# Kernel optimization log

Hardware: AMD Instinct MI355X
Metric: run time of the kernel (lower is better)

## Reference

```python
import jax, jax.numpy as jnp
import numpy as np

B, L, C = 2, 4096, 1024
H, WIN = 16, 128            # num_heads, window_size (each side)
D = C // H                  # head_dim = 64


def setup_inputs() -> dict:
    key = jax.random.key(0)
    ks = jax.random.split(key, 9)
    s = 0.02
    return {
        "x": jax.random.normal(ks[0], (B, L, C), jnp.float32),
        # Linear weights stored as [in, out] (y = x @ W + b), same math as torch Linear.
        "wq": jax.random.normal(ks[1], (C, C), jnp.float32) * s,
        "bq": jnp.zeros((C,), jnp.float32),
        "wk": jax.random.normal(ks[2], (C, C), jnp.float32) * s,
        "bk": jnp.zeros((C,), jnp.float32),
        "wv": jax.random.normal(ks[3], (C, C), jnp.float32) * s,
        "bv": jnp.zeros((C,), jnp.float32),
        "wo": jax.random.normal(ks[4], (C, C), jnp.float32) * s,
        "bo": jnp.zeros((C,), jnp.float32),
    }


def reference(x, wq, bq, wk, bk, wv, bv, wo, bo):
    b, l, c = x.shape
    nb = l // WIN

    def heads(t):  # (B,L,C) -> (B,H,L,D)
        return t.reshape(b, l, H, D).transpose(0, 2, 1, 3)

    q = heads(x @ wq + bq)
    k = heads(x @ wk + bk)
    v = heads(x @ wv + bv)

    # and ARE included in the softmax, exactly as the original module does).
    kp = jnp.pad(k, ((0, 0), (0, 0), (WIN, WIN), (0, 0)))
    vp = jnp.pad(v, ((0, 0), (0, 0), (WIN, WIN), (0, 0)))

    idx = np.arange(nb)[:, None] * WIN + np.arange(3 * WIN)[None, :]  # [nb, 3W]
    kb = kp[:, :, idx]  # [B,H,nb,3W,D]
    vb = vp[:, :, idx]  # [B,H,nb,3W,D]
    qb = q.reshape(b, H, nb, WIN, D)

    scores = jnp.einsum('bhnqd,bhnkd->bhnqk', qb, kb) / float(np.sqrt(D))
    r = np.arange(WIN)[:, None]
    col = np.arange(3 * WIN)[None, :]
    band = jnp.asarray(np.abs(col - r - WIN) <= WIN)
    scores = jnp.where(band, scores, -jnp.inf)
    probs = jax.nn.softmax(scores, axis=-1)

    out = jnp.einsum('bhnqk,bhnkd->bhnqd', probs, vb)
    out = out.reshape(b, H, l, D).transpose(0, 2, 1, 3).reshape(b, l, c)
    return out @ wo + bo
```

## Files before the change

### kernel.cpp

```cpp
#include <hip/hip_runtime.h>

using short8  = __attribute__((ext_vector_type(8))) short;
using short4v = __attribute__((ext_vector_type(4))) short;
using floatx4 = __attribute__((ext_vector_type(4))) float;

#define MFMA_B16(a, b, c) __builtin_amdgcn_mfma_f32_16x16x32_bf16(a, b, c, 0, 0, 0)

__device__ __forceinline__ short f2bf(float f) {
  union { float f; unsigned u; } v; v.f = f;
  unsigned r = v.u + 0x7fffu + ((v.u >> 16) & 1u);
  return (short)(r >> 16);
}
__device__ __forceinline__ short f2bf_rtz(float f) {
  union { float f; unsigned u; } v; v.f = f;
  return (short)(v.u >> 16);
}

__device__ __forceinline__ void gload_lds16(const short* g, short* l) {
  __builtin_amdgcn_global_load_lds(
      (const __attribute__((address_space(1))) unsigned int*)g,
      (__attribute__((address_space(3))) unsigned int*)l, 16, 0, 0);
}

__global__ __launch_bounds__(256) void prep(
    const float4* __restrict__ x, short4v* __restrict__ xb,
    const float* __restrict__ w0, const float* __restrict__ w1,
    const float* __restrict__ w2, const float* __restrict__ w3,
    short* __restrict__ wT) {
  __shared__ float tile[32][33];
  int blk = blockIdx.x;
  if (blk < 8192) {
    int i = blk * 256 + threadIdx.x;
    float4 v = x[i];
    short4v o = { f2bf(v.x), f2bf(v.y), f2bf(v.z), f2bf(v.w) };
    xb[i] = o;
  } else {
    int r = blk - 8192;
    int z = r >> 10; r &= 1023;
    const float* w = z == 0 ? w0 : (z == 1 ? w1 : (z == 2 ? w2 : w3));
    short* out = wT + (size_t)z * 1024 * 1024;
    int n0 = (r & 31) * 32, k0 = (r >> 5) * 32;
    int tx = threadIdx.x & 31, ty = threadIdx.x >> 5;
#pragma unroll
    for (int i = 0; i < 4; ++i)
      tile[ty + i * 8][tx] = w[(size_t)(k0 + ty + i * 8) * 1024 + n0 + tx];
    __syncthreads();
#pragma unroll
    for (int i = 0; i < 4; ++i)
      out[(size_t)(n0 + ty + i * 8) * 1024 + k0 + tx] = f2bf(tile[tx][ty + i * 8]);
  }
}

__global__ __launch_bounds__(256) void gemm_qkv(
    const short* __restrict__ xb, const short* __restrict__ wT,
    const float* __restrict__ bq, const float* __restrict__ bk,
    const float* __restrict__ bv, short* __restrict__ qkv) {
  const int K = 1024;
  int z = blockIdx.z;
  const short* wt = wT + (size_t)z * 1024 * 1024;
  const float* bias = z == 0 ? bq : (z == 1 ? bk : bv);
  short* out = qkv + (size_t)z * 8192 * 1024;

  int m0 = blockIdx.x * 128, n0 = blockIdx.y * 128;
  __shared__ __align__(16) short a[128][32];
  __shared__ __align__(16) short bt[128][32];
  int tid = threadIdx.x;
  int w = tid >> 6, lane = tid & 63, quad = lane >> 4, l16 = lane & 15;
  int wm = (w >> 1) * 64, wn = (w & 1) * 64;
  floatx4 zf = {0.f, 0.f, 0.f, 0.f};
  floatx4 acc[4][4];
#pragma unroll
  for (int i = 0; i < 4; ++i)
#pragma unroll
    for (int j = 0; j < 4; ++j) acc[i][j] = zf;

  int rowL = lane >> 2;
  int segL = (lane & 3) * 8;
  const short* ga = xb + (size_t)(m0 + w * 32 + rowL) * K + segL;
  const short* gb = wt + (size_t)(n0 + w * 32 + rowL) * K + segL;
  short* la = &a[w * 32][0];
  short* lb = &bt[w * 32][0];

  for (int k0 = 0; k0 < K; k0 += 32) {
    __syncthreads();
    gload_lds16(ga + k0, la);
    gload_lds16(ga + (size_t)16 * K + k0, la + 16 * 32);
    gload_lds16(gb + k0, lb);
    gload_lds16(gb + (size_t)16 * K + k0, lb + 16 * 32);
    __syncthreads();
    short8 af[4], bf[4];
#pragma unroll
    for (int t = 0; t < 4; ++t) {
      af[t] = *(const short8*)(&a[wm + t * 16 + l16][quad * 8]);
      bf[t] = *(const short8*)(&bt[wn + t * 16 + l16][quad * 8]);
    }
#pragma unroll
    for (int i = 0; i < 4; ++i)
#pragma unroll
      for (int j = 0; j < 4; ++j)
        acc[i][j] = MFMA_B16(af[i], bf[j], acc[i][j]);
  }

  float qs = (z == 0) ? 0.125f * 1.44269504f : 1.0f;
#pragma unroll
  for (int i = 0; i < 4; ++i)
#pragma unroll
    for (int j = 0; j < 4; ++j)
#pragma unroll
      for (int rg = 0; rg < 4; ++rg) {
        int m = m0 + wm + i * 16 + quad * 4 + rg;
        int cc = n0 + wn + j * 16 + l16;
        float v = (acc[i][j][rg] + bias[cc]) * qs;
        int b = m >> 12, l = m & 4095;
        int hh = cc >> 6, d = cc & 63;
        out[((size_t)(b * 16 + hh) * 4096 + l) * 64 + d] = f2bf(v);
      }
}

__global__ __launch_bounds__(256) void attn_kern(const short* __restrict__ qkv,
                                                 short* __restrict__ attnb) {
  const int L = 4096, H = 16;
  int n = blockIdx.x, h = blockIdx.y, b = blockIdx.z;
  const size_t hs = (size_t)L * 64;
  const short* Qp = qkv + (size_t)(b * H + h) * hs;
  const short* Kp = qkv + (size_t)8192 * 1024 + (size_t)(b * H + h) * hs;
  const short* Vp = qkv + (size_t)2 * 8192 * 1024 + (size_t)(b * H + h) * hs;

  __shared__ __align__(16) short kt[128][72];
  __shared__ __align__(16) short vt[64][136];
  __shared__ __align__(16) short pl[4][32][136];

  int tid = threadIdx.x, w = tid >> 6, lane = tid & 63, quad = lane >> 4, l16 = lane & 15;

  short8 onesf;
  {
    short ov = (l16 == 0) ? (short)0x3F80 : (short)0;
#pragma unroll
    for (int j = 0; j < 8; ++j) onesf[j] = ov;
  }

  short8 qf[2][2];
#pragma unroll
  for (int rt = 0; rt < 2; ++rt)
#pragma unroll
    for (int ks = 0; ks < 2; ++ks)
      qf[rt][ks] = *(const short8*)(Qp + (size_t)(n * 128 + w * 32 + rt * 16 + l16) * 64 + ks * 32 + quad * 8);

  floatx4 zf = {0.f, 0.f, 0.f, 0.f};
  floatx4 o[2][4];
  floatx4 osum[2];
#pragma unroll
  for (int i = 0; i < 2; ++i) {
    osum[i] = zf;
#pragma unroll
    for (int j = 0; j < 4; ++j) o[i][j] = zf;
  }

#pragma unroll
  for (int c = 0; c < 3; ++c) {
    int bk = n - 1 + c;
    bool inr = (c == 1) || (c == 0 ? (n > 0) : (n < 31));
    __syncthreads();
    if (inr) {
      const short* kc_ = Kp + (size_t)bk * 128 * 64;
      int kr = tid >> 2, ksg = (tid & 3) * 16;
#pragma unroll
      for (int p = 0; p < 2; ++p) {
        int r2 = p * 64 + kr;
        *(short8*)(&kt[r2][ksg])     = *(const short8*)(kc_ + r2 * 64 + ksg);
        *(short8*)(&kt[r2][ksg + 8]) = *(const short8*)(kc_ + r2 * 64 + ksg + 8);
      }
      const short* vc_ = Vp + (size_t)bk * 128 * 64;
      int vkey = tid & 31, vsg = (tid >> 5) * 8;
#pragma unroll
      for (int p = 0; p < 4; ++p) {
        int r2 = p * 32 + vkey;
        short8 vv = *(const short8*)(vc_ + r2 * 64 + vsg);
#pragma unroll
        for (int j = 0; j < 8; ++j) vt[vsg + j][r2] = vv[j];
      }
    } else {
      short8 z8 = {0, 0, 0, 0, 0, 0, 0, 0};
      int kr = tid >> 2, ksg = (tid & 3) * 16;
#pragma unroll
      for (int p = 0; p < 2; ++p) {
        int r2 = p * 64 + kr;
        *(short8*)(&kt[r2][ksg])     = z8;
        *(short8*)(&kt[r2][ksg + 8]) = z8;
      }
      int vr = tid >> 2, vsg2 = (tid & 3) * 32;
#pragma unroll
      for (int q2 = 0; q2 < 4; ++q2) *(short8*)(&vt[vr][vsg2 + q2 * 8]) = z8;
    }
    __syncthreads();

    floatx4 s[2][8];
#pragma unroll
    for (int rt = 0; rt < 2; ++rt)
#pragma unroll
      for (int ct = 0; ct < 8; ++ct) s[rt][ct] = zf;
#pragma unroll
    for (int ct = 0; ct < 8; ++ct) {
      bool any = (c == 0) ? (ct >= w * 2) : (c == 2) ? (ct <= w * 2 + 1) : true;
      if (any) {
        short8 kf0 = *(const short8*)(&kt[ct * 16 + l16][quad * 8]);
        short8 kf1 = *(const short8*)(&kt[ct * 16 + l16][32 + quad * 8]);
#pragma unroll
        for (int rt = 0; rt < 2; ++rt) {
          bool valid = (c == 0) ? (ct >= w * 2 + rt) : (c == 2) ? (ct <= w * 2 + rt) : true;
          if (valid) {
            s[rt][ct] = MFMA_B16(qf[rt][0], kf0, s[rt][ct]);
            s[rt][ct] = MFMA_B16(qf[rt][1], kf1, s[rt][ct]);
          }
        }
      }
    }

#pragma unroll
    for (int rt = 0; rt < 2; ++rt) {
      int wrt = w * 2 + rt;
#pragma unroll
      for (int ct = 0; ct < 8; ++ct) {
        bool tileMasked = (c == 0) ? (ct < wrt) : (c == 2) ? (ct > wrt) : false;
        bool ksDead = (c == 0) ? (2 * (ct >> 1) + 1 < wrt)
                    : (c == 2) ? (2 * (ct >> 1) > wrt) : false;
        bool diag = (c != 1) && (ct == wrt);
        if (ksDead) continue;
        if (tileMasked) {
#pragma unroll
          for (int rg = 0; rg < 4; ++rg)
            pl[w][rt * 16 + quad * 4 + rg][ct * 16 + l16] = 0;
        } else if (diag) {
#pragma unroll
          for (int rg = 0; rg < 4; ++rg) {
            int r16 = quad * 4 + rg;
            float p = exp2f(s[rt][ct][rg]);
            if (c == 0) p = (l16 < r16) ? 0.f : p;
            else        p = (l16 > r16) ? 0.f : p;
            pl[w][rt * 16 + r16][ct * 16 + l16] = f2bf_rtz(p);
          }
        } else {
#pragma unroll
          for (int rg = 0; rg < 4; ++rg)
            pl[w][rt * 16 + quad * 4 + rg][ct * 16 + l16] = f2bf_rtz(exp2f(s[rt][ct][rg]));
        }
      }
    }

    __syncthreads();

#pragma unroll
    for (int ks = 0; ks < 4; ++ks) {
      bool anyrt = (c == 0) ? (2 * ks + 1 >= w * 2) : (c == 2) ? (2 * ks <= w * 2 + 1) : true;
      if (!anyrt) continue;
      short8 vf[4];
#pragma unroll
      for (int ct = 0; ct < 4; ++ct)
        vf[ct] = *(const short8*)(&vt[ct * 16 + l16][ks * 32 + quad * 8]);
#pragma unroll
      for (int rt = 0; rt < 2; ++rt) {
        int wrt = w * 2 + rt;
        bool ksDead = (c == 0) ? (2 * ks + 1 < wrt) : (c == 2) ? (2 * ks > wrt) : false;
        if (ksDead) continue;
        short8 pf = *(const short8*)(&pl[w][rt * 16 + l16][ks * 32 + quad * 8]);
#pragma unroll
        for (int ct = 0; ct < 4; ++ct) o[rt][ct] = MFMA_B16(pf, vf[ct], o[rt][ct]);
        osum[rt] = MFMA_B16(pf, onesf, osum[rt]);
      }
    }
  }

#pragma unroll
  for (int rt = 0; rt < 2; ++rt) {
#pragma unroll
    for (int rg = 0; rg < 4; ++rg) {
      float ssum = __shfl(osum[rt][rg], lane & 48);
      float inv = 1.f / ssum;
      int r = n * 128 + w * 32 + rt * 16 + quad * 4 + rg;
#pragma unroll
      for (int ct = 0; ct < 4; ++ct)
        attnb[(size_t)(b * L + r) * 1024 + h * 64 + ct * 16 + l16] =
            f2bf(o[rt][ct][rg] * inv);
    }
  }
}

__global__ __launch_bounds__(256) void gemm_out(
    const short* __restrict__ attnb, const short* __restrict__ wTo,
    const float* __restrict__ bo, float* __restrict__ outp) {
  const int K = 1024;
  int m0 = blockIdx.x * 128, n0 = blockIdx.y * 128;
  __shared__ __align__(16) short a[128][32];
  __shared__ __align__(16) short bt[128][32];
  int tid = threadIdx.x;
  int w = tid >> 6, lane = tid & 63, quad = lane >> 4, l16 = lane & 15;
  int wm = (w >> 1) * 64, wn = (w & 1) * 64;
  floatx4 zf = {0.f, 0.f, 0.f, 0.f};
  floatx4 acc[4][4];
#pragma unroll
  for (int i = 0; i < 4; ++i)
#pragma unroll
    for (int j = 0; j < 4; ++j) acc[i][j] = zf;

  int rowL = lane >> 2;
  int segL = (lane & 3) * 8;
  const short* ga = attnb + (size_t)(m0 + w * 32 + rowL) * K + segL;
  const short* gb = wTo + (size_t)(n0 + w * 32 + rowL) * K + segL;
  short* la = &a[w * 32][0];
  short* lb = &bt[w * 32][0];

  for (int k0 = 0; k0 < K; k0 += 32) {
    __syncthreads();
    gload_lds16(ga + k0, la);
    gload_lds16(ga + (size_t)16 * K + k0, la + 16 * 32);
    gload_lds16(gb + k0, lb);
    gload_lds16(gb + (size_t)16 * K + k0, lb + 16 * 32);
    __syncthreads();
    short8 af[4], bf[4];
#pragma unroll
    for (int t = 0; t < 4; ++t) {
      af[t] = *(const short8*)(&a[wm + t * 16 + l16][quad * 8]);
      bf[t] = *(const short8*)(&bt[wn + t * 16 + l16][quad * 8]);
    }
#pragma unroll
    for (int i = 0; i < 4; ++i)
#pragma unroll
      for (int j = 0; j < 4; ++j)
        acc[i][j] = MFMA_B16(af[i], bf[j], acc[i][j]);
  }
#pragma unroll
  for (int i = 0; i < 4; ++i)
#pragma unroll
    for (int j = 0; j < 4; ++j)
#pragma unroll
      for (int rg = 0; rg < 4; ++rg) {
        int m = m0 + wm + i * 16 + quad * 4 + rg;
        int c = n0 + wn + j * 16 + l16;
        outp[(size_t)m * 1024 + c] = acc[i][j][rg] + bo[c];
      }
}

extern "C" void kernel_launch(void* const* d_in, const int* in_sizes, int n_in,
                              void* d_out, int out_size, void* d_ws, size_t ws_size,
                              hipStream_t stream) {
  const float* x  = (const float*)d_in[0];
  const float* wq = (const float*)d_in[1];
  const float* bq = (const float*)d_in[2];
  const float* wk = (const float*)d_in[3];
  const float* bk = (const float*)d_in[4];
  const float* wv = (const float*)d_in[5];
  const float* bv = (const float*)d_in[6];
  const float* wo = (const float*)d_in[7];
  const float* bo = (const float*)d_in[8];

  char* ws = (char*)d_ws;
  short* xb    = (short*)ws;
  short* wT    = (short*)(ws + (16u << 20));
  short* qkv   = (short*)(ws + (24u << 20));
  short* attnb = (short*)(ws + (72u << 20));

  prep<<<12288, 256, 0, stream>>>((const float4*)x, (short4v*)xb, wq, wk, wv, wo, wT);
  gemm_qkv<<<dim3(64, 8, 3), 256, 0, stream>>>(xb, wT, bq, bk, bv, qkv);
  attn_kern<<<dim3(32, 16, 2), 256, 0, stream>>>(qkv, attnb);
  gemm_out<<<dim3(64, 8), 256, 0, stream>>>(attnb, wT + 3u * 1024 * 1024, bo, (float*)d_out);
}
```

Before: 223.0 us.

## Replace GEMM kernels with double-buffered 256x128 pipelined MFMA core

Both projection GEMMs now share a 256x128-tile core run by 512 threads (8 waves). It uses BK=64, double-buffered LDS filled through direct global-to-LDS loads, and XOR swizzling to avoid bank conflicts. Loads are interleaved with MFMA halves under explicit waitcnt and barrier control, plus setprio around the math. The goal is to hide global latency and raise MFMA utilisation compared with the old single-buffered 128x128 BK=32 loop. The cost is more LDS (96KB per block) and fragile hand-tuned vmcnt counts.

```diff
diff --git a/kernel.cpp b/kernel.cpp
--- a/kernel.cpp
+++ b/kernel.cpp
@@ -51,66 +51,135 @@
   }
 }
 
-__global__ __launch_bounds__(256) void gemm_qkv(
+__device__ __forceinline__ void gemm_core_256x128(
+    const short* __restrict__ Ag0, const short* __restrict__ Bg0,
+    short* As , short* Bs ,
+    floatx4 (&acc)[8][2]) {
+  const int tid = threadIdx.x;
+  const int w = tid >> 6, lane = tid & 63, quad = lane >> 4, l16 = lane & 15;
+  const int wm = w >> 2, wn = w & 3;
+  const int srow = tid >> 3;
+  const int scol = ((tid & 7) ^ (srow & 7)) * 8;
+
+  floatx4 zf = {0.f, 0.f, 0.f, 0.f};
+#pragma unroll
+  for (int i = 0; i < 8; ++i) { acc[i][0] = zf; acc[i][1] = zf; }
+
+  const short* gA = Ag0 + (size_t)srow * 1024 + scol;
+  const short* gB = Bg0 + (size_t)srow * 1024 + scol;
+
+  auto stA = [&](int buf, int q, int kt) {
+    gload_lds16(gA + (size_t)q * 64 * 1024 + kt * 64,
+                As + buf * 16384 + q * 4096 + w * 512);
+  };
+  auto stB = [&](int buf, int q, int kt) {
+    gload_lds16(gB + (size_t)q * 64 * 1024 + kt * 64,
+                Bs + buf * 8192 + q * 4096 + w * 512);
+  };
+
+  short8 aF[8], bF[4];
+  auto ldA = [&](int buf, int mh) {
+    const char* base = (const char*)(As + buf * 16384);
+#pragma unroll
+    for (int m = 0; m < 4; ++m)
+#pragma unroll
+      for (int kk = 0; kk < 2; ++kk) {
+        int row = wm * 128 + mh * 64 + m * 16 + l16;
+        int off = row * 128 + kk * 64 + quad * 16;
+        off ^= (row & 7) << 4;
+        aF[m * 2 + kk] = *(const short8*)(base + off);
+      }
+  };
+  auto ldB = [&](int buf) {
+    const char* base = (const char*)(Bs + buf * 8192);
+#pragma unroll
+    for (int nf = 0; nf < 2; ++nf)
+#pragma unroll
+      for (int kk = 0; kk < 2; ++kk) {
+        int row = wn * 32 + nf * 16 + l16;
+        int off = row * 128 + kk * 64 + quad * 16;
+        off ^= (row & 7) << 4;
+        bF[nf * 2 + kk] = *(const short8*)(base + off);
+      }
+  };
+  auto mm = [&](int mh) {
+#pragma unroll
+    for (int m = 0; m < 4; ++m)
+#pragma unroll
+      for (int nf = 0; nf < 2; ++nf)
+#pragma unroll
+        for (int kk = 0; kk < 2; ++kk)
+          acc[mh * 4 + m][nf] =
+              MFMA_B16(aF[m * 2 + kk], bF[nf * 2 + kk], acc[mh * 4 + m][nf]);
+  };
+
+  stA(0, 0, 0); stA(0, 1, 0); stA(0, 2, 0); stA(0, 3, 0);
+  stB(0, 0, 0); stB(0, 1, 0);
+  stA(1, 0, 1); stA(1, 2, 1); stB(1, 0, 1);
+  asm volatile("s_waitcnt vmcnt(3)" ::: "memory");
+  __builtin_amdgcn_s_barrier();
+
+#pragma unroll 2
+  for (int t = 0; t < 16; ++t) {
+    const int cb = t & 1, nb = cb ^ 1;
+    ldA(cb, 0);
+    ldB(cb);
+    if (t + 1 < 16) { stA(nb, 1, t + 1); stA(nb, 3, t + 1); stB(nb, 1, t + 1); }
+    __builtin_amdgcn_sched_barrier(0);
+    __builtin_amdgcn_s_barrier();
+    asm volatile("s_waitcnt lgkmcnt(0)" ::: "memory");
+    __builtin_amdgcn_sched_barrier(0);
+    __builtin_amdgcn_s_setprio(1);
+    mm(0);
+    __builtin_amdgcn_s_setprio(0);
+    __builtin_amdgcn_sched_barrier(0);
+    __builtin_amdgcn_s_barrier();
+    ldA(cb, 1);
+    if (t + 2 < 16) {
+      stA(cb, 0, t + 2); stA(cb, 2, t + 2); stB(cb, 0, t + 2);
+      asm volatile("s_waitcnt vmcnt(3)" ::: "memory");
+    } else {
+      asm volatile("s_waitcnt vmcnt(0)" ::: "memory");
+    }
+    __builtin_amdgcn_sched_barrier(0);
+    __builtin_amdgcn_s_barrier();
+    asm volatile("s_waitcnt lgkmcnt(0)" ::: "memory");
+    __builtin_amdgcn_sched_barrier(0);
+    __builtin_amdgcn_s_setprio(1);
+    mm(1);
+    __builtin_amdgcn_s_setprio(0);
+    __builtin_amdgcn_sched_barrier(0);
+    __builtin_amdgcn_s_barrier();
+  }
+}
+
+__global__ __launch_bounds__(512, 2) void gemm_qkv(
     const short* __restrict__ xb, const short* __restrict__ wT,
     const float* __restrict__ bq, const float* __restrict__ bk,
     const float* __restrict__ bv, short* __restrict__ qkv) {
-  const int K = 1024;
+  __shared__ __align__(16) short As[2 * 16384];
+  __shared__ __align__(16) short Bs[2 * 8192];
   int z = blockIdx.z;
   const short* wt = wT + (size_t)z * 1024 * 1024;
   const float* bias = z == 0 ? bq : (z == 1 ? bk : bv);
   short* out = qkv + (size_t)z * 8192 * 1024;
-
-  int m0 = blockIdx.x * 128, n0 = blockIdx.y * 128;
-  __shared__ __align__(16) short a[128][32];
-  __shared__ __align__(16) short bt[128][32];
-  int tid = threadIdx.x;
-  int w = tid >> 6, lane = tid & 63, quad = lane >> 4, l16 = lane & 15;
-  int wm = (w >> 1) * 64, wn = (w & 1) * 64;
-  floatx4 zf = {0.f, 0.f, 0.f, 0.f};
-  floatx4 acc[4][4];
-#pragma unroll
-  for (int i = 0; i < 4; ++i)
-#pragma unroll
-    for (int j = 0; j < 4; ++j) acc[i][j] = zf;
-
-  int rowL = lane >> 2;
-  int segL = (lane & 3) * 8;
-  const short* ga = xb + (size_t)(m0 + w * 32 + rowL) * K + segL;
-  const short* gb = wt + (size_t)(n0 + w * 32 + rowL) * K + segL;
-  short* la = &a[w * 32][0];
-  short* lb = &bt[w * 32][0];
-
-  for (int k0 = 0; k0 < K; k0 += 32) {
-    __syncthreads();
-    gload_lds16(ga + k0, la);
-    gload_lds16(ga + (size_t)16 * K + k0, la + 16 * 32);
-    gload_lds16(gb + k0, lb);
-    gload_lds16(gb + (size_t)16 * K + k0, lb + 16 * 32);
-    __syncthreads();
-    short8 af[4], bf[4];
-#pragma unroll
-    for (int t = 0; t < 4; ++t) {
-      af[t] = *(const short8*)(&a[wm + t * 16 + l16][quad * 8]);
-      bf[t] = *(const short8*)(&bt[wn + t * 16 + l16][quad * 8]);
-    }
-#pragma unroll
-    for (int i = 0; i < 4; ++i)
-#pragma unroll
-      for (int j = 0; j < 4; ++j)
-        acc[i][j] = MFMA_B16(af[i], bf[j], acc[i][j]);
-  }
-
+  int m0 = blockIdx.x * 256, n0 = blockIdx.y * 128;
+
+  floatx4 acc[8][2];
+  gemm_core_256x128(xb + (size_t)m0 * 1024, wt + (size_t)n0 * 1024, As, Bs, acc);
+
+  int tid = threadIdx.x, w = tid >> 6, lane = tid & 63, quad = lane >> 4, l16 = lane & 15;
+  int wm = w >> 2, wn = w & 3;
   float qs = (z == 0) ? 0.125f * 1.44269504f : 1.0f;
 #pragma unroll
-  for (int i = 0; i < 4; ++i)
-#pragma unroll
-    for (int j = 0; j < 4; ++j)
+  for (int mf = 0; mf < 8; ++mf)
+#pragma unroll
+    for (int nf = 0; nf < 2; ++nf)
 #pragma unroll
       for (int rg = 0; rg < 4; ++rg) {
-        int m = m0 + wm + i * 16 + quad * 4 + rg;
-        int cc = n0 + wn + j * 16 + l16;
-        float v = (acc[i][j][rg] + bias[cc]) * qs;
+        int m = m0 + wm * 128 + mf * 16 + quad * 4 + rg;
+        int cc = n0 + wn * 32 + nf * 16 + l16;
+        float v = (acc[mf][nf][rg] + bias[cc]) * qs;
         int b = m >> 12, l = m & 4095;
         int hh = cc >> 6, d = cc & 63;
         out[((size_t)(b * 16 + hh) * 4096 + l) * 64 + d] = f2bf(v);
@@ -285,58 +354,27 @@
   }
 }
 
-__global__ __launch_bounds__(256) void gemm_out(
+__global__ __launch_bounds__(512, 2) void gemm_out(
     const short* __restrict__ attnb, const short* __restrict__ wTo,
     const float* __restrict__ bo, float* __restrict__ outp) {
-  const int K = 1024;
-  int m0 = blockIdx.x * 128, n0 = blockIdx.y * 128;
-  __shared__ __align__(16) short a[128][32];
-  __shared__ __align__(16) short bt[128][32];
-  int tid = threadIdx.x;
-  int w = tid >> 6, lane = tid & 63, quad = lane >> 4, l16 = lane & 15;
-  int wm = (w >> 1) * 64, wn = (w & 1) * 64;
-  floatx4 zf = {0.f, 0.f, 0.f, 0.f};
-  floatx4 acc[4][4];
-#pragma unroll
-  for (int i = 0; i < 4; ++i)
-#pragma unroll
-    for (int j = 0; j < 4; ++j) acc[i][j] = zf;
-
-  int rowL = lane >> 2;
-  int segL = (lane & 3) * 8;
-  const short* ga = attnb + (size_t)(m0 + w * 32 + rowL) * K + segL;
-  const short* gb = wTo + (size_t)(n0 + w * 32 + rowL) * K + segL;
-  short* la = &a[w * 32][0];
-  short* lb = &bt[w * 32][0];
-
-  for (int k0 = 0; k0 < K; k0 += 32) {
-    __syncthreads();
-    gload_lds16(ga + k0, la);
-    gload_lds16(ga + (size_t)16 * K + k0, la + 16 * 32);
-    gload_lds16(gb + k0, lb);
-    gload_lds16(gb + (size_t)16 * K + k0, lb + 16 * 32);
-    __syncthreads();
-    short8 af[4], bf[4];
-#pragma unroll
-    for (int t = 0; t < 4; ++t) {
-      af[t] = *(const short8*)(&a[wm + t * 16 + l16][quad * 8]);
-      bf[t] = *(const short8*)(&bt[wn + t * 16 + l16][quad * 8]);
-    }
-#pragma unroll
-    for (int i = 0; i < 4; ++i)
-#pragma unroll
-      for (int j = 0; j < 4; ++j)
-        acc[i][j] = MFMA_B16(af[i], bf[j], acc[i][j]);
-  }
-#pragma unroll
-  for (int i = 0; i < 4; ++i)
-#pragma unroll
-    for (int j = 0; j < 4; ++j)
+  __shared__ __align__(16) short As[2 * 16384];
+  __shared__ __align__(16) short Bs[2 * 8192];
+  int m0 = blockIdx.x * 256, n0 = blockIdx.y * 128;
+
+  floatx4 acc[8][2];
+  gemm_core_256x128(attnb + (size_t)m0 * 1024, wTo + (size_t)n0 * 1024, As, Bs, acc);
+
+  int tid = threadIdx.x, w = tid >> 6, lane = tid & 63, quad = lane >> 4, l16 = lane & 15;
+  int wm = w >> 2, wn = w & 3;
+#pragma unroll
+  for (int mf = 0; mf < 8; ++mf)
+#pragma unroll
+    for (int nf = 0; nf < 2; ++nf)
 #pragma unroll
       for (int rg = 0; rg < 4; ++rg) {
-        int m = m0 + wm + i * 16 + quad * 4 + rg;
-        int c = n0 + wn + j * 16 + l16;
-        outp[(size_t)m * 1024 + c] = acc[i][j][rg] + bo[c];
+        int m = m0 + wm * 128 + mf * 16 + quad * 4 + rg;
+        int cc = n0 + wn * 32 + nf * 16 + l16;
+        outp[(size_t)m * 1024 + cc] = acc[mf][nf][rg] + bo[cc];
       }
 }
 
@@ -360,7 +398,7 @@
   short* attnb = (short*)(ws + (72u << 20));
 
   prep<<<12288, 256, 0, stream>>>((const float4*)x, (short4v*)xb, wq, wk, wv, wo, wT);
-  gemm_qkv<<<dim3(64, 8, 3), 256, 0, stream>>>(xb, wT, bq, bk, bv, qkv);
+  gemm_qkv<<<dim3(32, 8, 3), 512, 0, stream>>>(xb, wT, bq, bk, bv, qkv);
   attn_kern<<<dim3(32, 16, 2), 256, 0, stream>>>(qkv, attnb);
-  gemm_out<<<dim3(64, 8), 256, 0, stream>>>(attnb, wT + 3u * 1024 * 1024, bo, (float*)d_out);
-}
+  gemm_out<<<dim3(32, 8), 512, 0, stream>>>(attnb, wT + 3u * 1024 * 1024, bo, (float*)d_out);
+}
```

Result: no change. 226.8 us (+1.7%).
